# Performance work log

Hardware: AMD Instinct MI355X
Metric: run time of the kernel (lower is better)

## Reference

```python
import jax, jax.numpy as jnp
import numpy as np

N = 50000        # nodes
E = 400000       # edges
IN_DIM = 128
HID = 64         # out_channels per head (concat=False -> mean over heads)
H = 4            # heads
C = HID          # per-head channels
HC = H * C
L = 6            # layers
EDIM = HID // 4  # edge embedding dim
NEG_SLOPE = 0.2


def setup_inputs() -> dict:
    key = jax.random.key(0)
    ks = jax.random.split(key, 16)
    s = 0.05
    return {
        "x": jax.random.normal(ks[0], (N, IN_DIM), dtype=jnp.float32),
        "edge_index": jax.random.randint(ks[1], (2, E), 0, N),
        "edge_attr": jax.random.randint(ks[2], (E,), 0, 3),
        "in_W": jax.random.normal(ks[3], (HID, IN_DIM), dtype=jnp.float32) * s,
        "in_b": jnp.zeros((HID,), jnp.float32),
        "edge_table": jax.random.normal(ks[4], (3, EDIM), dtype=jnp.float32) * s,
        "Wl": jax.random.normal(ks[5], (L, HC, HID), dtype=jnp.float32) * s,
        "bl": jnp.zeros((L, HC), jnp.float32),
        "Wr": jax.random.normal(ks[6], (L, HC, HID), dtype=jnp.float32) * s,
        "br": jnp.zeros((L, HC), jnp.float32),
        "We": jax.random.normal(ks[7], (L, HC, EDIM), dtype=jnp.float32) * s,
        "att": jax.random.normal(ks[8], (L, H, C), dtype=jnp.float32) * s,
        "out_bias": jnp.zeros((L, HID), jnp.float32),
        "ln_g": jnp.ones((L, HID), jnp.float32),
        "ln_b": jnp.zeros((L, HID), jnp.float32),
    }


def _layernorm(h, g, b):
    mu = h.mean(-1, keepdims=True)
    var = ((h - mu) ** 2).mean(-1, keepdims=True)
    return (h - mu) / jnp.sqrt(var + 1e-5) * g + b


def _gatv2_layer(h, src, dst, eemb, Wl, bl, Wr, br, We, att, bias):
    # GATv2Conv (PyG semantics, concat=False -> mean over heads), eval mode
    xl = (h @ Wl.T + bl).reshape(N, H, C)   # lin_l(x) -> source messages
    xr = (h @ Wr.T + br).reshape(N, H, C)   # lin_r(x) -> target term
    ep = (eemb @ We.T).reshape(E, H, C)     # lin_edge(edge_attr)
    m = xl[src] + xr[dst] + ep              # [E,H,C]
    s = jax.nn.leaky_relu(m, NEG_SLOPE)
    logit = jnp.einsum('ehc,hc->eh', s, att)  # [E,H]
    # segment softmax over incoming edges of each dst node
    mx = jax.ops.segment_max(logit, dst, num_segments=N)
    mx = jnp.where(jnp.isfinite(mx), mx, 0.0)
    ex = jnp.exp(logit - mx[dst])
    den = jax.ops.segment_sum(ex, dst, num_segments=N)
    alpha = ex / jnp.maximum(den[dst], 1e-16)           # [E,H]
    agg = jax.ops.segment_sum(xl[src] * alpha[:, :, None], dst, num_segments=N)  # [N,H,C]
    return agg.mean(axis=1) + bias          # concat=False -> head mean, then bias


def reference(x, edge_index, edge_attr, in_W, in_b, edge_table, Wl, bl, Wr, br,
              We, att, out_bias, ln_g, ln_b):
    h = x @ in_W.T + in_b                   # input projection [N,HID]
    eemb = edge_table[edge_attr]            # [E,EDIM]
    src, dst = edge_index[0], edge_index[1]
    use_res = [False] * (L // 2) + [True] * (L // 2)
    for i in range(L):
        h_in = h
        h = _gatv2_layer(h, src, dst, eemb, Wl[i], bl[i], Wr[i], br[i],
                         We[i], att[i], out_bias[i])
        h = _layernorm(h, ln_g[i], ln_b[i])
        if use_res[i]:
            h = h + h_in
        if i < L - 1:
            h = jax.nn.relu(h)  # dropout is identity in eval mode
    return h
```

## Files before the change

kernel.cpp:

```cpp
#include <hip/hip_runtime.h>
#include <hip/hip_bf16.h>
#include <hip/hip_fp16.h>
#include <math.h>

#define NN 50000
#define NE 400000
#define INDIM 128
#define HID 64
#define HC 256
#define NL 6
#define ED 16
#define SCAN_B 256
#define SCAN_NB ((NN + SCAN_B - 1)/SCAN_B)
#define NBIN 64
#define BINPAD 16

typedef __attribute__((ext_vector_type(8))) short short8;
typedef __attribute__((ext_vector_type(4))) float f32x4;
typedef _Float16 h2 __attribute__((ext_vector_type(2)));

static __device__ __forceinline__ float4 ld4(const float* p){ return *(const float4*)p; }
static __device__ __forceinline__ unsigned short f2b(float x){
  __hip_bfloat16 h = __float2bfloat16(x);
  return *(unsigned short*)&h;
}
static __device__ __forceinline__ unsigned short f2h(float x){
  __half h = __float2half(x);
  return *(unsigned short*)&h;
}

#define DPP_ADD(X, CTRL) \
  ((X) + __builtin_bit_cast(float, __builtin_amdgcn_update_dpp(0, __builtin_bit_cast(int, (X)), (CTRL), 0xF, 0xF, true)))

__global__ void prep_kernel(const float* __restrict__ inW, const float* __restrict__ Wl,
                            const float* __restrict__ Wr, const float* __restrict__ bl,
                            const float* __restrict__ br, const float* __restrict__ etab,
                            const float* __restrict__ We,
                            unsigned short* __restrict__ inW_bf,
                            unsigned short* __restrict__ Wlr,
                            float* __restrict__ blr, float* __restrict__ ep){
  int i = blockIdx.x*blockDim.x + threadIdx.x;
  if (i < HID*INDIM) inW_bf[i] = f2b(inW[i]);
  if (i < NL*512){
    int l = i / 512, c = i % 512;
    blr[i] = (c < HC) ? bl[l*HC + c] : br[l*HC + (c-HC)];
  }
  if (i < NL*3*HC){
    int l  = i / (3*HC);
    int a  = (i / HC) % 3;
    int hc = i % HC;
    const float* wrow = We + ((size_t)l*HC + hc)*ED;
    const float* erow = etab + a*ED;
    float s = 0.f;
    #pragma unroll
    for (int k=0;k<ED;k++) s += erow[k]*wrow[k];
    ep[i] = s;
  }
  int tot = NL*512*HID;
  for (int j = i; j < tot; j += gridDim.x*blockDim.x){
    int l = j / (512*HID);
    int c = (j / HID) % 512;
    int k = j % HID;
    float v = (c < HC) ? Wl[((size_t)l*HC + c)*HID + k]
                       : Wr[((size_t)l*HC + (c-HC))*HID + k];
    Wlr[j] = f2b(v);
  }
}

__global__ void deg_kernel(const int* __restrict__ dst, int* __restrict__ deg){
  int e = blockIdx.x*blockDim.x + threadIdx.x;
  if (e < NE) atomicAdd(&deg[dst[e]], 1);
}

__global__ void scanA_kernel(const int* __restrict__ deg, int* __restrict__ bsum){
  int t = threadIdx.x;
  int i = blockIdx.x*SCAN_B + t;
  int v = (i < NN) ? deg[i] : 0;
  #pragma unroll
  for (int o=1;o<64;o<<=1) v += __shfl_xor(v,o);
  __shared__ int ws[4];
  if ((t&63)==0) ws[t>>6] = v;
  __syncthreads();
  if (t==0) bsum[blockIdx.x] = ws[0]+ws[1]+ws[2]+ws[3];
}

__global__ void scanB_kernel(int* __restrict__ bsum){
  __shared__ int sh[256];
  int t = threadIdx.x;
  int v = (t < SCAN_NB) ? bsum[t] : 0;
  sh[t] = v;
  __syncthreads();
  for (int o=1;o<256;o<<=1){
    int u = (t>=o)?sh[t-o]:0;
    __syncthreads();
    sh[t]+=u;
    __syncthreads();
  }
  int excl = (t==0)?0:sh[t-1];
  if (t < SCAN_NB) bsum[t] = excl;
}

__global__ void scanC_kernel(const int* __restrict__ deg, const int* __restrict__ bsum,
                             int* __restrict__ rowp){
  int t = threadIdx.x, b = blockIdx.x;
  int i = b*SCAN_B + t;
  int v = (i<NN)?deg[i]:0;
  __shared__ int sh[256];
  sh[t]=v;
  __syncthreads();
  for (int o=1;o<256;o<<=1){
    int u=(t>=o)?sh[t-o]:0;
    __syncthreads();
    sh[t]+=u;
    __syncthreads();
  }
  if (i < NN) rowp[i] = bsum[b] + sh[t] - v;
  if (i == 0) rowp[NN] = NE;
}

__global__ void scatter_kernel(const int* __restrict__ src, const int* __restrict__ dst,
                               const int* __restrict__ attr, const int* __restrict__ rowp,
                               int* __restrict__ deg, int* __restrict__ csrp){
  int e = blockIdx.x*blockDim.x + threadIdx.x;
  if (e >= NE) return;
  int d = dst[e];
  int pos = rowp[d] + atomicSub(&deg[d], 1) - 1;
  csrp[pos] = src[e] | (attr[e] << 16);
}

__global__ void histE_kernel(const int* __restrict__ rowp, int* __restrict__ gbin,
                             int* __restrict__ bbase){
  __shared__ int lh[NBIN];
  int t = threadIdx.x, b = blockIdx.x;
  if (t < NBIN) lh[t] = 0;
  __syncthreads();
  int i = b*SCAN_B + t;
  if (i < NN){
    int dg = rowp[i+1] - rowp[i];
    if (dg > 63) dg = 63;
    atomicAdd(&lh[63 - dg], 1);
  }
  __syncthreads();
  if (t < NBIN){
    int c = lh[t];
    bbase[b*NBIN + t] = c ? atomicAdd(&gbin[t*BINPAD], c) : 0;
  }
}
__global__ void scanE_kernel(int* __restrict__ gbin){
  int t = threadIdx.x;
  int v = gbin[t*BINPAD];
  int s = v;
  #pragma unroll
  for (int o=1;o<64;o<<=1){
    int u = __shfl_up(s, o);
    if (t >= o) s += u;
  }
  gbin[t*BINPAD] = s - v;
}
__global__ void scatterE_kernel(const int* __restrict__ rowp, const int* __restrict__ gbin,
                                const int* __restrict__ bbase, int* __restrict__ order){
  __shared__ int lc[NBIN];
  int t = threadIdx.x, b = blockIdx.x;
  if (t < NBIN) lc[t] = 0;
  __syncthreads();
  int i = b*SCAN_B + t;
  if (i < NN){
    int dg = rowp[i+1] - rowp[i];
    if (dg > 63) dg = 63;
    int bin = 63 - dg;
    int r = atomicAdd(&lc[bin], 1);
    order[gbin[bin*BINPAD] + bbase[b*NBIN + bin] + r] = i;
  }
}

__global__ __launch_bounds__(256) void gemm_in_kernel(
    const float* __restrict__ X, const unsigned short* __restrict__ Wbf,
    const float* __restrict__ bias, float* __restrict__ hout, unsigned short* __restrict__ hbf)
{
  int wid = threadIdx.x >> 6, lane = threadIdx.x & 63;
  int row0 = blockIdx.x*128 + wid*32;
  int lr = lane & 15, lk = lane >> 4;
  short8 a[2][4];
  #pragma unroll
  for (int rt=0; rt<2; rt++){
    int r = row0 + rt*16 + lr; if (r >= NN) r = NN-1;
    const float* rp = X + (size_t)r*INDIM;
    #pragma unroll
    for (int ks=0; ks<4; ks++){
      const float* p = rp + ks*32 + lk*8;
      float4 u = ld4(p), v = ld4(p+4);
      short8 t;
      t[0]=(short)f2b(u.x); t[1]=(short)f2b(u.y); t[2]=(short)f2b(u.z); t[3]=(short)f2b(u.w);
      t[4]=(short)f2b(v.x); t[5]=(short)f2b(v.y); t[6]=(short)f2b(v.z); t[7]=(short)f2b(v.w);
      a[rt][ks] = t;
    }
  }
  f32x4 acc[2][4] = {};
  #pragma unroll
  for (int ct=0; ct<4; ct++){
    int c = ct*16 + lr;
    #pragma unroll
    for (int ks=0; ks<4; ks++){
      short8 b = *(const short8*)&Wbf[(size_t)c*INDIM + ks*32 + lk*8];
      #pragma unroll
      for (int rt=0; rt<2; rt++)
        acc[rt][ct] = __builtin_amdgcn_mfma_f32_16x16x32_bf16(a[rt][ks], b, acc[rt][ct], 0,0,0);
    }
  }
  #pragma unroll
  for (int rt=0; rt<2; rt++)
    #pragma unroll
    for (int ct=0; ct<4; ct++){
      int c = ct*16 + lr;
      float bv = bias[c];
      #pragma unroll
      for (int q=0;q<4;q++){
        int r = row0 + rt*16 + lk*4 + q;
        if (r < NN){
          float v = acc[rt][ct][q] + bv;
          hout[(size_t)r*HID + c] = v;
          hbf[(size_t)r*HID + c] = f2b(v);
        }
      }
    }
}

__global__ __launch_bounds__(256) void gemm_lr_kernel(
    const unsigned short* __restrict__ Abf, const unsigned short* __restrict__ Wbf,
    const float* __restrict__ bias, unsigned short* __restrict__ out)
{
  int wid = threadIdx.x >> 6, lane = threadIdx.x & 63;
  int row0 = blockIdx.x*128 + wid*32;
  int col0 = blockIdx.y*64;
  int lr = lane & 15, lk = lane >> 4;
  short8 a[2][2];
  #pragma unroll
  for (int rt=0; rt<2; rt++){
    int r = row0 + rt*16 + lr; if (r >= NN) r = NN-1;
    #pragma unroll
    for (int ks=0; ks<2; ks++)
      a[rt][ks] = *(const short8*)&Abf[(size_t)r*HID + ks*32 + lk*8];
  }
  f32x4 acc[2][4] = {};
  #pragma unroll
  for (int ct=0; ct<4; ct++){
    int c = col0 + ct*16 + lr;
    #pragma unroll
    for (int ks=0; ks<2; ks++){
      short8 b = *(const short8*)&Wbf[(size_t)c*HID + ks*32 + lk*8];
      #pragma unroll
      for (int rt=0; rt<2; rt++)
        acc[rt][ct] = __builtin_amdgcn_mfma_f32_16x16x32_bf16(a[rt][ks], b, acc[rt][ct], 0,0,0);
    }
  }
  #pragma unroll
  for (int rt=0; rt<2; rt++)
    #pragma unroll
    for (int ct=0; ct<4; ct++){
      int c = col0 + ct*16 + lr;
      float bv = bias[c];
      #pragma unroll
      for (int q=0;q<4;q++){
        int r = row0 + rt*16 + lk*4 + q;
        if (r < NN) out[(size_t)r*512 + c] = f2h(acc[rt][ct][q] + bv);
      }
    }
}

#define EDGE_BODY(UX, UY, A)                                                   \
  {                                                                            \
    h2 x2a = __builtin_bit_cast(h2, (UX));                                     \
    h2 x2b = __builtin_bit_cast(h2, (UY));                                     \
    h2 m2a = x2a + ((A)==0 ? xre0a : ((A)==1 ? xre1a : xre2a));                \
    h2 m2b = x2b + ((A)==0 ? xre0b : ((A)==1 ? xre1b : xre2b));                \
    h2 n2a = __builtin_bit_cast(h2, __builtin_bit_cast(unsigned, m2a) & 0x7FFF7FFFu); \
    h2 n2b = __builtin_bit_cast(h2, __builtin_bit_cast(unsigned, m2b) & 0x7FFF7FFFu); \
    float part = __builtin_amdgcn_fdot2(m2a, av6a, 0.f, false);                \
    part = __builtin_amdgcn_fdot2(m2b, av6b, part, false);                     \
    part = __builtin_amdgcn_fdot2(n2a, av4a, part, false);                     \
    part = __builtin_amdgcn_fdot2(n2b, av4b, part, false);                     \
    part = DPP_ADD(part, 0xB1);                                                \
    part = DPP_ADD(part, 0x4E);                                                \
    part = DPP_ADD(part, 0x124);                                               \
    part = DPP_ADD(part, 0x128);                                               \
    float p = exp2f(part);                                                     \
    den += p;                                                                  \
    ax = fmaf(p, (float)x2a.x, ax);                                            \
    ay = fmaf(p, (float)x2a.y, ay);                                            \
    az = fmaf(p, (float)x2b.x, az);                                            \
    aw = fmaf(p, (float)x2b.y, aw);                                            \
  }

__global__ __launch_bounds__(256) void agg_kernel(
    const unsigned short* __restrict__ xlr,
    const int* __restrict__ rowp, const int* __restrict__ csrp,
    const int* __restrict__ order,
    const float* __restrict__ ep_l, const float* __restrict__ att_l,
    const float* __restrict__ bias_l, const float* __restrict__ g_l, const float* __restrict__ b_l,
    const float* __restrict__ h_in, float* __restrict__ h_out, unsigned short* __restrict__ hbf,
    int use_res, int do_relu)
{
  int idx = (blockIdx.x << 2) | (threadIdx.x >> 6);
  int lane = threadIdx.x & 63;
  if (idx >= NN) return;
  int d = order[idx];
  int cb = lane << 2;

  uint2 xru = *(const uint2*)(xlr + ((size_t)d << 9) + 256 + cb);
  h2 xr2a = __builtin_bit_cast(h2, xru.x);
  h2 xr2b = __builtin_bit_cast(h2, xru.y);
  float xrf0 = (float)xr2a.x, xrf1 = (float)xr2a.y;
  float xrf2 = (float)xr2b.x, xrf3 = (float)xr2b.y;

  float4 ev0 = ld4(ep_l + cb);
  float4 ev1 = ld4(ep_l + HC + cb);
  float4 ev2 = ld4(ep_l + 2*HC + cb);
  h2 xre0a = {(_Float16)(xrf0+ev0.x), (_Float16)(xrf1+ev0.y)};
  h2 xre0b = {(_Float16)(xrf2+ev0.z), (_Float16)(xrf3+ev0.w)};
  h2 xre1a = {(_Float16)(xrf0+ev1.x), (_Float16)(xrf1+ev1.y)};
  h2 xre1b = {(_Float16)(xrf2+ev1.z), (_Float16)(xrf3+ev1.w)};
  h2 xre2a = {(_Float16)(xrf0+ev2.x), (_Float16)(xrf1+ev2.y)};
  h2 xre2b = {(_Float16)(xrf2+ev2.z), (_Float16)(xrf3+ev2.w)};

  float4 av = ld4(att_l + cb);
  const float K6 = 0.6f*1.44269504f, K4 = 0.4f*1.44269504f;
  h2 av6a = {(_Float16)(av.x*K6), (_Float16)(av.y*K6)};
  h2 av6b = {(_Float16)(av.z*K6), (_Float16)(av.w*K6)};
  h2 av4a = {(_Float16)(av.x*K4), (_Float16)(av.y*K4)};
  h2 av4b = {(_Float16)(av.z*K4), (_Float16)(av.w*K4)};

  float den = 0.f;
  float ax=0.f, ay=0.f, az=0.f, aw=0.f;

  int beg = rowp[d], stop = rowp[d+1];
  int i = beg;
  for (; i + 4 <= stop; i += 4){
    int p0 = csrp[i], p1 = csrp[i+1], p2 = csrp[i+2], p3 = csrp[i+3];
    uint2 u0 = *(const uint2*)(xlr + ((size_t)(p0 & 0xFFFF) << 9) + cb);
    uint2 u1 = *(const uint2*)(xlr + ((size_t)(p1 & 0xFFFF) << 9) + cb);
    uint2 u2 = *(const uint2*)(xlr + ((size_t)(p2 & 0xFFFF) << 9) + cb);
    uint2 u3 = *(const uint2*)(xlr + ((size_t)(p3 & 0xFFFF) << 9) + cb);
    int a0 = p0 >> 16, a1 = p1 >> 16, a2 = p2 >> 16, a3 = p3 >> 16;
    EDGE_BODY(u0.x, u0.y, a0);
    EDGE_BODY(u1.x, u1.y, a1);
    EDGE_BODY(u2.x, u2.y, a2);
    EDGE_BODY(u3.x, u3.y, a3);
  }
  if (i + 2 <= stop){
    int p0 = csrp[i], p1 = csrp[i+1];
    uint2 u0 = *(const uint2*)(xlr + ((size_t)(p0 & 0xFFFF) << 9) + cb);
    uint2 u1 = *(const uint2*)(xlr + ((size_t)(p1 & 0xFFFF) << 9) + cb);
    int a0 = p0 >> 16, a1 = p1 >> 16;
    EDGE_BODY(u0.x, u0.y, a0);
    EDGE_BODY(u1.x, u1.y, a1);
    i += 2;
  }
  if (i < stop){
    int p0 = csrp[i];
    uint2 u0 = *(const uint2*)(xlr + ((size_t)(p0 & 0xFFFF) << 9) + cb);
    int a0 = p0 >> 16;
    EDGE_BODY(u0.x, u0.y, a0);
  }

  float inv = (den > 0.f) ? 1.f/den : 0.f;
  ax *= inv; ay *= inv; az *= inv; aw *= inv;

  ax += __shfl_xor(ax,16); ay += __shfl_xor(ay,16); az += __shfl_xor(az,16); aw += __shfl_xor(aw,16);
  ax += __shfl_xor(ax,32); ay += __shfl_xor(ay,32); az += __shfl_xor(az,32); aw += __shfl_xor(aw,32);

  int cc = (lane & 15) << 2;
  float4 bv = ld4(bias_l + cc);
  float h0 = ax*0.25f + bv.x;
  float h1 = ay*0.25f + bv.y;
  float h2v = az*0.25f + bv.z;
  float h3 = aw*0.25f + bv.w;

  float s1 = h0+h1+h2v+h3;
  float s2 = h0*h0 + h1*h1 + h2v*h2v + h3*h3;
  s1 += __shfl_xor(s1,1); s2 += __shfl_xor(s2,1);
  s1 += __shfl_xor(s1,2); s2 += __shfl_xor(s2,2);
  s1 += __shfl_xor(s1,4); s2 += __shfl_xor(s2,4);
  s1 += __shfl_xor(s1,8); s2 += __shfl_xor(s2,8);
  float mu  = s1 * (1.f/64.f);
  float var = fmaxf(s2*(1.f/64.f) - mu*mu, 0.f);
  float rstd = rsqrtf(var + 1e-5f);
  float4 gv  = ld4(g_l + cc);
  float4 bbv = ld4(b_l + cc);
  float r0 = (h0-mu)*rstd*gv.x + bbv.x;
  float r1 = (h1-mu)*rstd*gv.y + bbv.y;
  float r2 = (h2v-mu)*rstd*gv.z + bbv.z;
  float r3 = (h3-mu)*rstd*gv.w + bbv.w;
  if (use_res){
    float4 hv = ld4(h_in + (size_t)d*HID + cc);
    r0 += hv.x; r1 += hv.y; r2 += hv.z; r3 += hv.w;
  }
  if (do_relu){
    r0 = fmaxf(r0, 0.f); r1 = fmaxf(r1, 0.f);
    r2 = fmaxf(r2, 0.f); r3 = fmaxf(r3, 0.f);
  }
  if (lane < 16){
    float4 o = {r0, r1, r2, r3};
    *(float4*)(h_out + (size_t)d*HID + cc) = o;
    ushort4 obv = {f2b(r0), f2b(r1), f2b(r2), f2b(r3)};
    *(ushort4*)(hbf + (size_t)d*HID + cc) = obv;
  }
}

extern "C" void kernel_launch(void* const* d_in, const int* in_sizes, int n_in,
                              void* d_out, int out_size, void* d_ws, size_t ws_size,
                              hipStream_t stream){
  const float* x    = (const float*)d_in[0];
  const int*   ei   = (const int*)d_in[1];
  const int*   ea   = (const int*)d_in[2];
  const float* inW  = (const float*)d_in[3];
  const float* inb  = (const float*)d_in[4];
  const float* etab = (const float*)d_in[5];
  const float* Wl   = (const float*)d_in[6];
  const float* bl   = (const float*)d_in[7];
  const float* Wr   = (const float*)d_in[8];
  const float* br   = (const float*)d_in[9];
  const float* We   = (const float*)d_in[10];
  const float* att  = (const float*)d_in[11];
  const float* ob   = (const float*)d_in[12];
  const float* lg   = (const float*)d_in[13];
  const float* lb   = (const float*)d_in[14];

  char* w = (char*)d_ws;
  size_t off = 0;
  auto alloc = [&](size_t bytes)->char*{
    char* p = w + off;
    off = (off + bytes + 255) & ~(size_t)255;
    return p;
  };
  float* hA    = (float*)alloc((size_t)NN*HID*4);
  float* hB    = (float*)alloc((size_t)NN*HID*4);
  unsigned short* hbf = (unsigned short*)alloc((size_t)NN*HID*2);
  unsigned short* xlr = (unsigned short*)alloc((size_t)NN*512*2);
  unsigned short* inW_bf = (unsigned short*)alloc((size_t)HID*INDIM*2);
  unsigned short* Wlr    = (unsigned short*)alloc((size_t)NL*512*HID*2);
  float* blr   = (float*)alloc((size_t)NL*512*4);
  float* ep    = (float*)alloc((size_t)NL*3*HC*4);
  int*   deg   = (int*)alloc((size_t)NN*4);
  int*   bsum  = (int*)alloc((size_t)SCAN_NB*4);
  int*   rowp  = (int*)alloc((size_t)(NN+1)*4);
  int*   csrp  = (int*)alloc((size_t)NE*4);
  int*   gbin  = (int*)alloc((size_t)NBIN*BINPAD*4);
  int*   bbase = (int*)alloc((size_t)SCAN_NB*NBIN*4);
  int*   order = (int*)alloc((size_t)NN*4);

  hipMemsetAsync(deg, 0, (size_t)NN*4, stream);
  hipMemsetAsync(gbin, 0, (size_t)NBIN*BINPAD*4, stream);

  const int* srcp = ei;
  const int* dstp = ei + NE;
  deg_kernel<<<dim3((NE+255)/256), dim3(256), 0, stream>>>(dstp, deg);
  scanA_kernel<<<dim3(SCAN_NB), dim3(256), 0, stream>>>(deg, bsum);
  scanB_kernel<<<dim3(1), dim3(256), 0, stream>>>(bsum);
  scanC_kernel<<<dim3(SCAN_NB), dim3(256), 0, stream>>>(deg, bsum, rowp);
  scatter_kernel<<<dim3((NE+255)/256), dim3(256), 0, stream>>>(srcp, dstp, ea, rowp, deg, csrp);
  histE_kernel<<<dim3(SCAN_NB), dim3(256), 0, stream>>>(rowp, gbin, bbase);
  scanE_kernel<<<dim3(1), dim3(64), 0, stream>>>(gbin);
  scatterE_kernel<<<dim3(SCAN_NB), dim3(256), 0, stream>>>(rowp, gbin, bbase, order);
  prep_kernel<<<dim3(64), dim3(256), 0, stream>>>(inW, Wl, Wr, bl, br, etab, We, inW_bf, Wlr, blr, ep);

  const int MB = (NN + 127)/128;
  gemm_in_kernel<<<dim3(MB), dim3(256), 0, stream>>>(x, inW_bf, inb, hA, hbf);

  float* hcur = hA; float* hnext = hB;
  for (int l=0; l<NL; l++){
    gemm_lr_kernel<<<dim3(MB,8), dim3(256), 0, stream>>>(
        hbf, Wlr + (size_t)l*512*HID, blr + (size_t)l*512, xlr);
    float* hout = (l == NL-1) ? (float*)d_out : hnext;
    agg_kernel<<<dim3((NN+3)/4), dim3(256), 0, stream>>>(
        xlr, rowp, csrp, order,
        ep + (size_t)l*3*HC, att + (size_t)l*HC,
        ob + (size_t)l*HID, lg + (size_t)l*HID, lb + (size_t)l*HID,
        hcur, hout, hbf, (l >= NL/2) ? 1 : 0, (l < NL-1) ? 1 : 0);
    float* t = hcur; hcur = hnext; hnext = t;
  }
}
```

Measured before the change: 547.0 us.

## Split wavefront into two half-waves processing two edges concurrently with 16B gathers

The aggregation kernel now has each half of the 64-lane wavefront handle a different incoming edge. Each lane covers 8 fp16 channels with a 16-byte gather instead of 4 channels with an 8-byte gather, so each edge-row load and its per-head reduction use fewer lanes and fewer DPP steps. The two half-wave partial sums are combined with a cross-half shuffle before normalization, and head-mean and LayerNorm reductions are remapped to the new lane layout. This aims to halve the serial per-edge iterations per node and widen memory transactions, at the cost of more registers and a masked weight on odd-degree tails.

Result: slower. 571.4 us (+4.5%).

```diff
diff --git a/kernel.cpp b/kernel.cpp
--- a/kernel.cpp
+++ b/kernel.cpp
@@ -27,6 +27,10 @@
 static __device__ __forceinline__ unsigned short f2h(float x){
   __half h = __float2half(x);
   return *(unsigned short*)&h;
+}
+static __device__ __forceinline__ h2 bch(unsigned u){ return __builtin_bit_cast(h2, u); }
+static __device__ __forceinline__ h2 hab(h2 x){
+  return __builtin_bit_cast(h2, __builtin_bit_cast(unsigned, x) & 0x7FFF7FFFu);
 }
 
 #define DPP_ADD(X, CTRL) \
@@ -267,29 +271,36 @@
     }
 }
 
-#define EDGE_BODY(UX, UY, A)                                                   \
+#define PBODY(P, U, WM)                                                        \
   {                                                                            \
-    h2 x2a = __builtin_bit_cast(h2, (UX));                                     \
-    h2 x2b = __builtin_bit_cast(h2, (UY));                                     \
-    h2 m2a = x2a + ((A)==0 ? xre0a : ((A)==1 ? xre1a : xre2a));                \
-    h2 m2b = x2b + ((A)==0 ? xre0b : ((A)==1 ? xre1b : xre2b));                \
-    h2 n2a = __builtin_bit_cast(h2, __builtin_bit_cast(unsigned, m2a) & 0x7FFF7FFFu); \
-    h2 n2b = __builtin_bit_cast(h2, __builtin_bit_cast(unsigned, m2b) & 0x7FFF7FFFu); \
-    float part = __builtin_amdgcn_fdot2(m2a, av6a, 0.f, false);                \
-    part = __builtin_amdgcn_fdot2(m2b, av6b, part, false);                     \
-    part = __builtin_amdgcn_fdot2(n2a, av4a, part, false);                     \
-    part = __builtin_amdgcn_fdot2(n2b, av4b, part, false);                     \
+    int a_ = (P) >> 16;                                                        \
+    h2 x0 = bch((U).x), x1 = bch((U).y), x2 = bch((U).z), x3 = bch((U).w);     \
+    h2 r0 = a_==0 ? xreA0 : (a_==1 ? xreB0 : xreC0);                           \
+    h2 r1 = a_==0 ? xreA1 : (a_==1 ? xreB1 : xreC1);                           \
+    h2 r2 = a_==0 ? xreA2 : (a_==1 ? xreB2 : xreC2);                           \
+    h2 r3 = a_==0 ? xreA3 : (a_==1 ? xreB3 : xreC3);                           \
+    h2 m0 = x0+r0, m1 = x1+r1, m2 = x2+r2, m3 = x3+r3;                         \
+    h2 n0 = hab(m0), n1 = hab(m1), n2 = hab(m2), n3 = hab(m3);                 \
+    float part = __builtin_amdgcn_fdot2(m0, av6_0, 0.f, false);                \
+    part = __builtin_amdgcn_fdot2(m1, av6_1, part, false);                     \
+    part = __builtin_amdgcn_fdot2(m2, av6_2, part, false);                     \
+    part = __builtin_amdgcn_fdot2(m3, av6_3, part, false);                     \
+    part = __builtin_amdgcn_fdot2(n0, av4_0, part, false);                     \
+    part = __builtin_amdgcn_fdot2(n1, av4_1, part, false);                     \
+    part = __builtin_amdgcn_fdot2(n2, av4_2, part, false);                     \
+    part = __builtin_amdgcn_fdot2(n3, av4_3, part, false);                     \
     part = DPP_ADD(part, 0xB1);                                                \
     part = DPP_ADD(part, 0x4E);                                                \
-    part = DPP_ADD(part, 0x124);                                               \
-    part = DPP_ADD(part, 0x128);                                               \
-    float p = exp2f(part);                                                     \
-    den += p;                                                                  \
-    ax = fmaf(p, (float)x2a.x, ax);                                            \
-    ay = fmaf(p, (float)x2a.y, ay);                                            \
-    az = fmaf(p, (float)x2b.x, az);                                            \
-    aw = fmaf(p, (float)x2b.y, aw);                                            \
-  }
+    part = DPP_ADD(part, 0x141);                                               \
+    float p_ = exp2f(part) * (WM);                                             \
+    den += p_;                                                                 \
+    a0f = fmaf(p_, (float)x0.x, a0f); a1f = fmaf(p_, (float)x0.y, a1f);        \
+    a2f = fmaf(p_, (float)x1.x, a2f); a3f = fmaf(p_, (float)x1.y, a3f);        \
+    a4f = fmaf(p_, (float)x2.x, a4f); a5f = fmaf(p_, (float)x2.y, a5f);        \
+    a6f = fmaf(p_, (float)x3.x, a6f); a7f = fmaf(p_, (float)x3.y, a7f);        \
+  }
+
+#define GATHER(P) (*(const uint4*)(xlr + (((size_t)((P) & 0xFFFF)) << 9) + c8))
 
 __global__ __launch_bounds__(256) void agg_kernel(
     const unsigned short* __restrict__ xlr,
@@ -304,105 +315,127 @@
   int lane = threadIdx.x & 63;
   if (idx >= NN) return;
   int d = order[idx];
-  int cb = lane << 2;
-
-  uint2 xru = *(const uint2*)(xlr + ((size_t)d << 9) + 256 + cb);
-  h2 xr2a = __builtin_bit_cast(h2, xru.x);
-  h2 xr2b = __builtin_bit_cast(h2, xru.y);
-  float xrf0 = (float)xr2a.x, xrf1 = (float)xr2a.y;
-  float xrf2 = (float)xr2b.x, xrf3 = (float)xr2b.y;
-
-  float4 ev0 = ld4(ep_l + cb);
-  float4 ev1 = ld4(ep_l + HC + cb);
-  float4 ev2 = ld4(ep_l + 2*HC + cb);
-  h2 xre0a = {(_Float16)(xrf0+ev0.x), (_Float16)(xrf1+ev0.y)};
-  h2 xre0b = {(_Float16)(xrf2+ev0.z), (_Float16)(xrf3+ev0.w)};
-  h2 xre1a = {(_Float16)(xrf0+ev1.x), (_Float16)(xrf1+ev1.y)};
-  h2 xre1b = {(_Float16)(xrf2+ev1.z), (_Float16)(xrf3+ev1.w)};
-  h2 xre2a = {(_Float16)(xrf0+ev2.x), (_Float16)(xrf1+ev2.y)};
-  h2 xre2b = {(_Float16)(xrf2+ev2.z), (_Float16)(xrf3+ev2.w)};
-
-  float4 av = ld4(att_l + cb);
+  int el = lane >> 5;
+  int q  = lane & 31;
+  int c8 = q << 3;
+
+  uint4 xru = *(const uint4*)(xlr + ((size_t)d << 9) + 256 + c8);
+  h2 xr0 = bch(xru.x), xr1 = bch(xru.y), xr2 = bch(xru.z), xr3 = bch(xru.w);
+  float xf0=(float)xr0.x, xf1=(float)xr0.y, xf2=(float)xr1.x, xf3=(float)xr1.y;
+  float xf4=(float)xr2.x, xf5=(float)xr2.y, xf6=(float)xr3.x, xf7=(float)xr3.y;
+
+  float4 eA0 = ld4(ep_l + c8),        eA1 = ld4(ep_l + c8 + 4);
+  float4 eB0 = ld4(ep_l + HC + c8),   eB1 = ld4(ep_l + HC + c8 + 4);
+  float4 eC0 = ld4(ep_l + 2*HC + c8), eC1 = ld4(ep_l + 2*HC + c8 + 4);
+  h2 xreA0 = {(_Float16)(xf0+eA0.x), (_Float16)(xf1+eA0.y)};
+  h2 xreA1 = {(_Float16)(xf2+eA0.z), (_Float16)(xf3+eA0.w)};
+  h2 xreA2 = {(_Float16)(xf4+eA1.x), (_Float16)(xf5+eA1.y)};
+  h2 xreA3 = {(_Float16)(xf6+eA1.z), (_Float16)(xf7+eA1.w)};
+  h2 xreB0 = {(_Float16)(xf0+eB0.x), (_Float16)(xf1+eB0.y)};
+  h2 xreB1 = {(_Float16)(xf2+eB0.z), (_Float16)(xf3+eB0.w)};
+  h2 xreB2 = {(_Float16)(xf4+eB1.x), (_Float16)(xf5+eB1.y)};
+  h2 xreB3 = {(_Float16)(xf6+eB1.z), (_Float16)(xf7+eB1.w)};
+  h2 xreC0 = {(_Float16)(xf0+eC0.x), (_Float16)(xf1+eC0.y)};
+  h2 xreC1 = {(_Float16)(xf2+eC0.z), (_Float16)(xf3+eC0.w)};
+  h2 xreC2 = {(_Float16)(xf4+eC1.x), (_Float16)(xf5+eC1.y)};
+  h2 xreC3 = {(_Float16)(xf6+eC1.z), (_Float16)(xf7+eC1.w)};
+
+  float4 av0 = ld4(att_l + c8), av1 = ld4(att_l + c8 + 4);
   const float K6 = 0.6f*1.44269504f, K4 = 0.4f*1.44269504f;
-  h2 av6a = {(_Float16)(av.x*K6), (_Float16)(av.y*K6)};
-  h2 av6b = {(_Float16)(av.z*K6), (_Float16)(av.w*K6)};
-  h2 av4a = {(_Float16)(av.x*K4), (_Float16)(av.y*K4)};
-  h2 av4b = {(_Float16)(av.z*K4), (_Float16)(av.w*K4)};
+  h2 av6_0 = {(_Float16)(av0.x*K6), (_Float16)(av0.y*K6)};
+  h2 av6_1 = {(_Float16)(av0.z*K6), (_Float16)(av0.w*K6)};
+  h2 av6_2 = {(_Float16)(av1.x*K6), (_Float16)(av1.y*K6)};
+  h2 av6_3 = {(_Float16)(av1.z*K6), (_Float16)(av1.w*K6)};
+  h2 av4_0 = {(_Float16)(av0.x*K4), (_Float16)(av0.y*K4)};
+  h2 av4_1 = {(_Float16)(av0.z*K4), (_Float16)(av0.w*K4)};
+  h2 av4_2 = {(_Float16)(av1.x*K4), (_Float16)(av1.y*K4)};
+  h2 av4_3 = {(_Float16)(av1.z*K4), (_Float16)(av1.w*K4)};
 
   float den = 0.f;
-  float ax=0.f, ay=0.f, az=0.f, aw=0.f;
+  float a0f=0.f,a1f=0.f,a2f=0.f,a3f=0.f,a4f=0.f,a5f=0.f,a6f=0.f,a7f=0.f;
 
   int beg = rowp[d], stop = rowp[d+1];
   int i = beg;
   for (; i + 4 <= stop; i += 4){
-    int p0 = csrp[i], p1 = csrp[i+1], p2 = csrp[i+2], p3 = csrp[i+3];
-    uint2 u0 = *(const uint2*)(xlr + ((size_t)(p0 & 0xFFFF) << 9) + cb);
-    uint2 u1 = *(const uint2*)(xlr + ((size_t)(p1 & 0xFFFF) << 9) + cb);
-    uint2 u2 = *(const uint2*)(xlr + ((size_t)(p2 & 0xFFFF) << 9) + cb);
-    uint2 u3 = *(const uint2*)(xlr + ((size_t)(p3 & 0xFFFF) << 9) + cb);
-    int a0 = p0 >> 16, a1 = p1 >> 16, a2 = p2 >> 16, a3 = p3 >> 16;
-    EDGE_BODY(u0.x, u0.y, a0);
-    EDGE_BODY(u1.x, u1.y, a1);
-    EDGE_BODY(u2.x, u2.y, a2);
-    EDGE_BODY(u3.x, u3.y, a3);
+    int pA = csrp[i + el];
+    int pB = csrp[i + 2 + el];
+    uint4 uA = GATHER(pA);
+    uint4 uB = GATHER(pB);
+    PBODY(pA, uA, 1.0f);
+    PBODY(pB, uB, 1.0f);
   }
   if (i + 2 <= stop){
-    int p0 = csrp[i], p1 = csrp[i+1];
-    uint2 u0 = *(const uint2*)(xlr + ((size_t)(p0 & 0xFFFF) << 9) + cb);
-    uint2 u1 = *(const uint2*)(xlr + ((size_t)(p1 & 0xFFFF) << 9) + cb);
-    int a0 = p0 >> 16, a1 = p1 >> 16;
-    EDGE_BODY(u0.x, u0.y, a0);
-    EDGE_BODY(u1.x, u1.y, a1);
+    int pA = csrp[i + el];
+    uint4 uA = GATHER(pA);
+    PBODY(pA, uA, 1.0f);
     i += 2;
   }
   if (i < stop){
-    int p0 = csrp[i];
-    uint2 u0 = *(const uint2*)(xlr + ((size_t)(p0 & 0xFFFF) << 9) + cb);
-    int a0 = p0 >> 16;
-    EDGE_BODY(u0.x, u0.y, a0);
-  }
-
-  float inv = (den > 0.f) ? 1.f/den : 0.f;
-  ax *= inv; ay *= inv; az *= inv; aw *= inv;
-
-  ax += __shfl_xor(ax,16); ay += __shfl_xor(ay,16); az += __shfl_xor(az,16); aw += __shfl_xor(aw,16);
-  ax += __shfl_xor(ax,32); ay += __shfl_xor(ay,32); az += __shfl_xor(az,32); aw += __shfl_xor(aw,32);
-
-  int cc = (lane & 15) << 2;
-  float4 bv = ld4(bias_l + cc);
-  float h0 = ax*0.25f + bv.x;
-  float h1 = ay*0.25f + bv.y;
-  float h2v = az*0.25f + bv.z;
-  float h3 = aw*0.25f + bv.w;
-
-  float s1 = h0+h1+h2v+h3;
-  float s2 = h0*h0 + h1*h1 + h2v*h2v + h3*h3;
-  s1 += __shfl_xor(s1,1); s2 += __shfl_xor(s2,1);
-  s1 += __shfl_xor(s1,2); s2 += __shfl_xor(s2,2);
-  s1 += __shfl_xor(s1,4); s2 += __shfl_xor(s2,4);
-  s1 += __shfl_xor(s1,8); s2 += __shfl_xor(s2,8);
+    int pA = csrp[i];
+    uint4 uA = GATHER(pA);
+    float wm = (el == 0) ? 1.0f : 0.0f;
+    PBODY(pA, uA, wm);
+  }
+
+  den += __shfl_xor(den, 32);
+  a0f += __shfl_xor(a0f, 32); a1f += __shfl_xor(a1f, 32);
+  a2f += __shfl_xor(a2f, 32); a3f += __shfl_xor(a3f, 32);
+  a4f += __shfl_xor(a4f, 32); a5f += __shfl_xor(a5f, 32);
+  a6f += __shfl_xor(a6f, 32); a7f += __shfl_xor(a7f, 32);
+
+  float inv = (den > 0.f) ? 0.25f/den : 0.f;
+  a0f*=inv; a1f*=inv; a2f*=inv; a3f*=inv; a4f*=inv; a5f*=inv; a6f*=inv; a7f*=inv;
+
+  a0f = DPP_ADD(a0f, 0x128); a0f += __shfl_xor(a0f, 16);
+  a1f = DPP_ADD(a1f, 0x128); a1f += __shfl_xor(a1f, 16);
+  a2f = DPP_ADD(a2f, 0x128); a2f += __shfl_xor(a2f, 16);
+  a3f = DPP_ADD(a3f, 0x128); a3f += __shfl_xor(a3f, 16);
+  a4f = DPP_ADD(a4f, 0x128); a4f += __shfl_xor(a4f, 16);
+  a5f = DPP_ADD(a5f, 0x128); a5f += __shfl_xor(a5f, 16);
+  a6f = DPP_ADD(a6f, 0x128); a6f += __shfl_xor(a6f, 16);
+  a7f = DPP_ADD(a7f, 0x128); a7f += __shfl_xor(a7f, 16);
+
+  int cc = (q & 7) << 3;
+  float4 bv0 = ld4(bias_l + cc), bv1 = ld4(bias_l + cc + 4);
+  float h0 = a0f + bv0.x, h1 = a1f + bv0.y, h2v = a2f + bv0.z, h3 = a3f + bv0.w;
+  float h4 = a4f + bv1.x, h5 = a5f + bv1.y, h6 = a6f + bv1.z, h7 = a7f + bv1.w;
+
+  float s1 = h0+h1+h2v+h3+h4+h5+h6+h7;
+  float s2 = h0*h0+h1*h1+h2v*h2v+h3*h3+h4*h4+h5*h5+h6*h6+h7*h7;
+  s1 = DPP_ADD(s1, 0xB1); s1 = DPP_ADD(s1, 0x4E); s1 = DPP_ADD(s1, 0x141);
+  s2 = DPP_ADD(s2, 0xB1); s2 = DPP_ADD(s2, 0x4E); s2 = DPP_ADD(s2, 0x141);
   float mu  = s1 * (1.f/64.f);
   float var = fmaxf(s2*(1.f/64.f) - mu*mu, 0.f);
   float rstd = rsqrtf(var + 1e-5f);
-  float4 gv  = ld4(g_l + cc);
-  float4 bbv = ld4(b_l + cc);
-  float r0 = (h0-mu)*rstd*gv.x + bbv.x;
-  float r1 = (h1-mu)*rstd*gv.y + bbv.y;
-  float r2 = (h2v-mu)*rstd*gv.z + bbv.z;
-  float r3 = (h3-mu)*rstd*gv.w + bbv.w;
+  float4 gv0 = ld4(g_l + cc), gv1 = ld4(g_l + cc + 4);
+  float4 bb0 = ld4(b_l + cc), bb1 = ld4(b_l + cc + 4);
+  float r0 = (h0-mu)*rstd*gv0.x + bb0.x;
+  float r1 = (h1-mu)*rstd*gv0.y + bb0.y;
+  float r2 = (h2v-mu)*rstd*gv0.z + bb0.z;
+  float r3 = (h3-mu)*rstd*gv0.w + bb0.w;
+  float r4 = (h4-mu)*rstd*gv1.x + bb1.x;
+  float r5 = (h5-mu)*rstd*gv1.y + bb1.y;
+  float r6 = (h6-mu)*rstd*gv1.z + bb1.z;
+  float r7 = (h7-mu)*rstd*gv1.w + bb1.w;
   if (use_res){
-    float4 hv = ld4(h_in + (size_t)d*HID + cc);
-    r0 += hv.x; r1 += hv.y; r2 += hv.z; r3 += hv.w;
+    float4 hv0 = ld4(h_in + (size_t)d*HID + cc);
+    float4 hv1 = ld4(h_in + (size_t)d*HID + cc + 4);
+    r0 += hv0.x; r1 += hv0.y; r2 += hv0.z; r3 += hv0.w;
+    r4 += hv1.x; r5 += hv1.y; r6 += hv1.z; r7 += hv1.w;
   }
   if (do_relu){
-    r0 = fmaxf(r0, 0.f); r1 = fmaxf(r1, 0.f);
-    r2 = fmaxf(r2, 0.f); r3 = fmaxf(r3, 0.f);
-  }
-  if (lane < 16){
-    float4 o = {r0, r1, r2, r3};
-    *(float4*)(h_out + (size_t)d*HID + cc) = o;
-    ushort4 obv = {f2b(r0), f2b(r1), f2b(r2), f2b(r3)};
-    *(ushort4*)(hbf + (size_t)d*HID + cc) = obv;
+    r0 = fmaxf(r0,0.f); r1 = fmaxf(r1,0.f); r2 = fmaxf(r2,0.f); r3 = fmaxf(r3,0.f);
+    r4 = fmaxf(r4,0.f); r5 = fmaxf(r5,0.f); r6 = fmaxf(r6,0.f); r7 = fmaxf(r7,0.f);
+  }
+  if (lane < 8){
+    float4 o0 = {r0, r1, r2, r3};
+    float4 o1 = {r4, r5, r6, r7};
+    *(float4*)(h_out + (size_t)d*HID + cc) = o0;
+    *(float4*)(h_out + (size_t)d*HID + cc + 4) = o1;
+    ushort4 ob0 = {f2b(r0), f2b(r1), f2b(r2), f2b(r3)};
+    ushort4 ob1 = {f2b(r4), f2b(r5), f2b(r6), f2b(r7)};
+    *(ushort4*)(hbf + (size_t)d*HID + cc) = ob0;
+    *(ushort4*)(hbf + (size_t)d*HID + cc + 4) = ob1;
   }
 }
 
```
